# Kernel optimization log

Measured on AMD Instinct MI355X. Metric: run time of the kernel, lower is better.

## Reference

```python
import jax, jax.numpy as jnp
import numpy as np

B, N, DIM, H, DH = 8, 1024, 512, 8, 64
INNER = H * DH
SCALE = DH ** -0.5
EPS = 1e-12  # F.normalize eps


def setup_inputs() -> dict:
    key = jax.random.key(0)
    k1, k2, k3, k4, k5 = jax.random.split(key, 5)
    x = jax.random.normal(k1, (B, N, DIM), dtype=jnp.float32)
    spd = jax.random.normal(k2, (B, 1, N, N), dtype=jnp.float32)
    # per-head binomial keep mask (one realized draw of the original loop), guaranteed nonzero
    a = np.random.RandomState(0).binomial(1, 0.9, size=H)
    if a.sum() == 0:
        a[0] = 1
    head_mask = jnp.asarray(a, dtype=jnp.float32)
    W_qkv = jax.random.normal(k3, (DIM, 3 * INNER), dtype=jnp.float32) * (DIM ** -0.5)
    W_out = jax.random.normal(k4, (INNER, DIM), dtype=jnp.float32) * (INNER ** -0.5)
    b_out = jax.random.normal(k5, (DIM,), dtype=jnp.float32) * 0.01
    return {"x": x, "spd": spd, "head_mask": head_mask,
            "W_qkv": W_qkv, "W_out": W_out, "b_out": b_out}


def reference(x, spd, head_mask, W_qkv, W_out, b_out):
    b, n, _ = x.shape
    qkv = x @ W_qkv                                   # [b, n, 3*inner]
    q, k, v = jnp.split(qkv, 3, axis=-1)
    split_heads = lambda t: t.reshape(b, n, H, DH).transpose(0, 2, 1, 3)  # b h n d
    q, k, v = split_heads(q), split_heads(k), split_heads(v)

    dots = jnp.einsum('bhnd,bhmd->bhnm', q, k) * SCALE        # [b,h,n,n]
    prod = dots * spd                                         # broadcast spd over heads
    prod_norm = jnp.sqrt(jnp.sum(prod * prod, axis=-1, keepdims=True))
    dots_norm = jnp.sqrt(jnp.sum(dots * dots, axis=-1, keepdims=True))
    bias = prod / jnp.maximum(prod_norm, EPS) * dots_norm     # F.normalize(prod)*||dots||
    attn = jax.nn.softmax(dots + bias, axis=-1)

    # head dropout mask with rescale: attn * mask * H / sum(mask)
    scale_m = head_mask * (H / jnp.sum(head_mask))
    attn = attn * scale_m[None, :, None, None]

    out = jnp.einsum('bhnm,bhmd->bhnd', attn, v)              # [b,h,n,d]
    out = out.transpose(0, 2, 1, 3).reshape(b, n, INNER)      # b n (h d)
    return out @ W_out + b_out
```

## Files before the change

kernel.cpp:

```cpp
#include <hip/hip_runtime.h>
#include <hip/hip_bf16.h>

typedef __attribute__((ext_vector_type(8))) short short8;
typedef __attribute__((ext_vector_type(4))) short s16x4;
typedef __attribute__((ext_vector_type(4))) float f32x4;
typedef __attribute__((ext_vector_type(2))) _Float16 h2;

typedef const __attribute__((address_space(1))) unsigned* gp1;
typedef __attribute__((address_space(3))) unsigned* lp3;

__device__ inline short f2bf(float f) {
    union { float f; unsigned u; } v; v.f = f;
    unsigned r = v.u + 0x7fffu + ((v.u >> 16) & 1u);
    return (short)(r >> 16);
}

__global__ __launch_bounds__(256) void cvt_bf16(
    const float* __restrict__ src, short* __restrict__ dst, int n4)
{
    int i = blockIdx.x * 256 + threadIdx.x;
    if (i < n4) {
        float4 v = ((const float4*)src)[i];
        s16x4 o = { f2bf(v.x), f2bf(v.y), f2bf(v.z), f2bf(v.w) };
        ((s16x4*)dst)[i] = o;
    }
}

__global__ __launch_bounds__(256) void tr_w(
    const float* __restrict__ src, short* __restrict__ dst, int K, int N)
{
    __shared__ float t[64][65];
    const int k0 = blockIdx.x * 64, n0 = blockIdx.y * 64;
    const int r = threadIdx.x >> 4, c4 = (threadIdx.x & 15) * 4;
#pragma unroll
    for (int j = 0; j < 4; j++) {
        float4 v = *(const float4*)(src + (size_t)(k0 + r + 16 * j) * N + n0 + c4);
        t[r + 16 * j][c4 + 0] = v.x; t[r + 16 * j][c4 + 1] = v.y;
        t[r + 16 * j][c4 + 2] = v.z; t[r + 16 * j][c4 + 3] = v.w;
    }
    __syncthreads();
#pragma unroll
    for (int j = 0; j < 4; j++) {
        const int n = r + 16 * j;
        s16x4 o = { f2bf(t[c4 + 0][n]), f2bf(t[c4 + 1][n]),
                    f2bf(t[c4 + 2][n]), f2bf(t[c4 + 3][n]) };
        *(s16x4*)(dst + (size_t)(n0 + n) * K + k0 + c4) = o;
    }
}

__global__ __launch_bounds__(256) void qkv_gemm(
    const short* __restrict__ A, const short* __restrict__ BT,
    short* __restrict__ q, short* __restrict__ k, short* __restrict__ vt)
{
    __shared__ short sA[128][32];
    __shared__ short sB[128][32];

    const int tid  = threadIdx.x;
    const int wv   = tid >> 6, lane = tid & 63;
    const int quad = lane >> 4, l16 = lane & 15;
    const int wr = wv >> 1, wc = wv & 1;
    const int m0 = blockIdx.x * 128, n0 = blockIdx.y * 128;

    f32x4 acc[4][4];
#pragma unroll
    for (int i = 0; i < 4; i++)
#pragma unroll
        for (int j = 0; j < 4; j++) acc[i][j] = (f32x4){0.f, 0.f, 0.f, 0.f};

    const short* a_src = A  + (size_t)(m0 + wv * 32 + (lane >> 2)) * 512 + (lane & 3) * 8;
    const short* b_src = BT + (size_t)(n0 + wv * 32 + (lane >> 2)) * 512 + (lane & 3) * 8;
    char* a_dst = (char*)sA + wv * 2048;
    char* b_dst = (char*)sB + wv * 2048;

    for (int ks = 0; ks < 16; ks++) {
        __syncthreads();
        const short* ap = a_src + ks * 32;
        const short* bp = b_src + ks * 32;
        __builtin_amdgcn_global_load_lds((gp1)(ap),            (lp3)(a_dst),        16, 0, 0);
        __builtin_amdgcn_global_load_lds((gp1)(ap + 16 * 512), (lp3)(a_dst + 1024), 16, 0, 0);
        __builtin_amdgcn_global_load_lds((gp1)(bp),            (lp3)(b_dst),        16, 0, 0);
        __builtin_amdgcn_global_load_lds((gp1)(bp + 16 * 512), (lp3)(b_dst + 1024), 16, 0, 0);
        __syncthreads();

        short8 af[4], bf[4];
#pragma unroll
        for (int f = 0; f < 4; f++) {
            af[f] = *(const short8*)&sA[wr * 64 + f * 16 + l16][quad * 8];
            bf[f] = *(const short8*)&sB[wc * 64 + f * 16 + l16][quad * 8];
        }
#pragma unroll
        for (int fm = 0; fm < 4; fm++)
#pragma unroll
            for (int fn = 0; fn < 4; fn++)
                acc[fm][fn] = __builtin_amdgcn_mfma_f32_16x16x32_bf16(
                    af[fm], bf[fn], acc[fm][fn], 0, 0, 0);
    }

    const int sec = n0 >> 9;
#pragma unroll
    for (int fn = 0; fn < 4; fn++) {
        const int gc = n0 + wc * 64 + fn * 16 + l16;
        const int cc = gc & 511;
        const int h = cc >> 6, d = cc & 63;
#pragma unroll
        for (int fm = 0; fm < 4; fm++)
#pragma unroll
            for (int i = 0; i < 4; i++) {
                const int gm = m0 + wr * 64 + fm * 16 + quad * 4 + i;
                const int b = gm >> 10, n = gm & 1023;
                const int bh = b * 8 + h;
                if (sec == 0)      q[((size_t)(bh * 1024 + n)) * 64 + d] = f2bf(acc[fm][fn][i] * 0.125f);
                else if (sec == 1) k[((size_t)(bh * 1024 + n)) * 64 + d] = f2bf(acc[fm][fn][i]);
                else               vt[((size_t)(bh * 64 + d)) * 1024 + n] = f2bf(acc[fm][fn][i]);
            }
    }
}

__global__ __launch_bounds__(256, 3) void attn_k(
    const short* __restrict__ q, const short* __restrict__ kk,
    const short* __restrict__ vt, const float* __restrict__ spd,
    const float* __restrict__ hm, short* __restrict__ o)
{
    __shared__ short sP[16][1032];
    __shared__ float sred[4][4][16];

    const int tid  = threadIdx.x;
    const int wv   = tid >> 6, lane = tid & 63;
    const int quad = lane >> 4, l16 = lane & 15;
    const int qt = blockIdx.x, bh = blockIdx.y;
    const int b = bh >> 3, h = bh & 7;
    const int q0 = qt * 16;

    const short* qb = q + ((size_t)bh * 1024 + q0 + l16) * 64;
    short8 aq0 = *(const short8*)(qb + quad * 8);
    short8 aq1 = *(const short8*)(qb + 32 + quad * 8);

    f32x4 acc[16];
#pragma unroll
    for (int t = 0; t < 16; t++) acc[t] = (f32x4){0.f, 0.f, 0.f, 0.f};

    const short* kbh = kk + (size_t)bh * 1024 * 64;
    const float* spdb = spd + ((size_t)b * 1024 + q0 + quad * 4) * 1024;

    h2 svp[16][2];

    float svfA[8][4];
#pragma unroll
    for (int t = 0; t < 8; t++) {
        const float* sp = spdb + wv * 256 + t * 16 + l16;
        svfA[t][0] = sp[0];    svfA[t][1] = sp[1024];
        svfA[t][2] = sp[2048]; svfA[t][3] = sp[3072];
    }
#pragma unroll
    for (int t = 0; t < 8; t++) {
        const short* kb = kbh + (size_t)(wv * 256 + t * 16 + l16) * 64;
        short8 b0 = *(const short8*)(kb + quad * 8);
        short8 b1 = *(const short8*)(kb + 32 + quad * 8);
        acc[t] = __builtin_amdgcn_mfma_f32_16x16x32_bf16(aq0, b0, acc[t], 0, 0, 0);
        acc[t] = __builtin_amdgcn_mfma_f32_16x16x32_bf16(aq1, b1, acc[t], 0, 0, 0);
    }
#pragma unroll
    for (int t = 0; t < 8; t++) {
        svp[t][0] = (h2){(_Float16)svfA[t][0], (_Float16)svfA[t][1]};
        svp[t][1] = (h2){(_Float16)svfA[t][2], (_Float16)svfA[t][3]};
    }
    float svfB[8][4];
#pragma unroll
    for (int t = 0; t < 8; t++) {
        const float* sp = spdb + wv * 256 + (t + 8) * 16 + l16;
        svfB[t][0] = sp[0];    svfB[t][1] = sp[1024];
        svfB[t][2] = sp[2048]; svfB[t][3] = sp[3072];
    }
#pragma unroll
    for (int t = 8; t < 16; t++) {
        const short* kb = kbh + (size_t)(wv * 256 + t * 16 + l16) * 64;
        short8 b0 = *(const short8*)(kb + quad * 8);
        short8 b1 = *(const short8*)(kb + 32 + quad * 8);
        acc[t] = __builtin_amdgcn_mfma_f32_16x16x32_bf16(aq0, b0, acc[t], 0, 0, 0);
        acc[t] = __builtin_amdgcn_mfma_f32_16x16x32_bf16(aq1, b1, acc[t], 0, 0, 0);
    }
#pragma unroll
    for (int t = 0; t < 8; t++) {
        svp[t + 8][0] = (h2){(_Float16)svfB[t][0], (_Float16)svfB[t][1]};
        svp[t + 8][1] = (h2){(_Float16)svfB[t][2], (_Float16)svfB[t][3]};
    }

    float dn[4] = {0.f, 0.f, 0.f, 0.f}, pn[4] = {0.f, 0.f, 0.f, 0.f};
#pragma unroll
    for (int t = 0; t < 16; t++)
#pragma unroll
        for (int i = 0; i < 4; i++) {
            float s  = acc[t][i];
            float sv = (float)svp[t][i >> 1][i & 1];
            float ps = s * sv;
            dn[i] += s * s;
            pn[i] += ps * ps;
        }
#pragma unroll
    for (int m = 1; m < 16; m <<= 1)
#pragma unroll
        for (int i = 0; i < 4; i++) {
            dn[i] += __shfl_xor(dn[i], m, 64);
            pn[i] += __shfl_xor(pn[i], m, 64);
        }
    if (l16 == 0)
#pragma unroll
        for (int i = 0; i < 4; i++) {
            sred[0][wv][quad * 4 + i] = dn[i];
            sred[1][wv][quad * 4 + i] = pn[i];
        }
    __syncthreads();
    float ratio[4];
#pragma unroll
    for (int i = 0; i < 4; i++) {
        const int row = quad * 4 + i;
        float d = sred[0][0][row] + sred[0][1][row] + sred[0][2][row] + sred[0][3][row];
        float p = sred[1][0][row] + sred[1][1][row] + sred[1][2][row] + sred[1][3][row];
        ratio[i] = sqrtf(d) / fmaxf(sqrtf(p), 1e-12f);
    }

    float mx[4] = {-1e30f, -1e30f, -1e30f, -1e30f};
#pragma unroll
    for (int t = 0; t < 16; t++)
#pragma unroll
        for (int i = 0; i < 4; i++) {
            float s  = acc[t][i];
            float sv = (float)svp[t][i >> 1][i & 1];
            float l  = s * fmaf(sv, ratio[i], 1.0f);
            acc[t][i] = l;
            mx[i] = fmaxf(mx[i], l);
        }
#pragma unroll
    for (int m = 1; m < 16; m <<= 1)
#pragma unroll
        for (int i = 0; i < 4; i++) mx[i] = fmaxf(mx[i], __shfl_xor(mx[i], m, 64));
    if (l16 == 0)
#pragma unroll
        for (int i = 0; i < 4; i++) sred[2][wv][quad * 4 + i] = mx[i];
    __syncthreads();
    float mrow[4];
#pragma unroll
    for (int i = 0; i < 4; i++) {
        const int row = quad * 4 + i;
        mrow[i] = fmaxf(fmaxf(sred[2][0][row], sred[2][1][row]),
                        fmaxf(sred[2][2][row], sred[2][3][row]));
    }

    float rs[4] = {0.f, 0.f, 0.f, 0.f};
#pragma unroll
    for (int t = 0; t < 16; t++)
#pragma unroll
        for (int i = 0; i < 4; i++) {
            float p = __expf(acc[t][i] - mrow[i]);
            acc[t][i] = p;
            rs[i] += p;
        }
#pragma unroll
    for (int m = 1; m < 16; m <<= 1)
#pragma unroll
        for (int i = 0; i < 4; i++) rs[i] += __shfl_xor(rs[i], m, 64);
    if (l16 == 0)
#pragma unroll
        for (int i = 0; i < 4; i++) sred[3][wv][quad * 4 + i] = rs[i];
    __syncthreads();
    const float hsum = hm[0] + hm[1] + hm[2] + hm[3] + hm[4] + hm[5] + hm[6] + hm[7];
    const float hscale = hm[h] * 8.0f / hsum;
    float rinv[4];
#pragma unroll
    for (int i = 0; i < 4; i++) {
        const int row = quad * 4 + i;
        float s = sred[3][0][row] + sred[3][1][row] + sred[3][2][row] + sred[3][3][row];
        rinv[i] = hscale / s;
    }

#pragma unroll
    for (int t = 0; t < 16; t++) {
        const int col = wv * 256 + t * 16 + l16;
#pragma unroll
        for (int i = 0; i < 4; i++)
            sP[quad * 4 + i][col] = f2bf(acc[t][i] * rinv[i]);
    }
    __syncthreads();

    f32x4 oacc = (f32x4){0.f, 0.f, 0.f, 0.f};
    const short* vb = vt + ((size_t)bh * 64 + wv * 16 + l16) * 1024;
#pragma unroll
    for (int kkk = 0; kkk < 32; kkk++) {
        short8 pa = *(const short8*)&sP[l16][kkk * 32 + quad * 8];
        short8 vf = *(const short8*)(vb + kkk * 32 + quad * 8);
        oacc = __builtin_amdgcn_mfma_f32_16x16x32_bf16(pa, vf, oacc, 0, 0, 0);
    }
#pragma unroll
    for (int i = 0; i < 4; i++)
        o[((size_t)(b * 1024 + q0 + quad * 4 + i)) * 512 + h * 64 + wv * 16 + l16]
            = f2bf(oacc[i]);
}

__global__ __launch_bounds__(256) void out_gemm(
    const short* __restrict__ A, const short* __restrict__ BT,
    const float* __restrict__ bias, float* __restrict__ out)
{
    __shared__ short sA[128][32];
    __shared__ short sB[128][32];

    const int tid  = threadIdx.x;
    const int wv   = tid >> 6, lane = tid & 63;
    const int quad = lane >> 4, l16 = lane & 15;
    const int wr = wv >> 1, wc = wv & 1;
    const int m0 = blockIdx.x * 128, n0 = blockIdx.y * 128;

    f32x4 acc[4][4];
#pragma unroll
    for (int i = 0; i < 4; i++)
#pragma unroll
        for (int j = 0; j < 4; j++) acc[i][j] = (f32x4){0.f, 0.f, 0.f, 0.f};

    const short* a_src = A  + (size_t)(m0 + wv * 32 + (lane >> 2)) * 512 + (lane & 3) * 8;
    const short* b_src = BT + (size_t)(n0 + wv * 32 + (lane >> 2)) * 512 + (lane & 3) * 8;
    char* a_dst = (char*)sA + wv * 2048;
    char* b_dst = (char*)sB + wv * 2048;

    for (int ks = 0; ks < 16; ks++) {
        __syncthreads();
        const short* ap = a_src + ks * 32;
        const short* bp = b_src + ks * 32;
        __builtin_amdgcn_global_load_lds((gp1)(ap),            (lp3)(a_dst),        16, 0, 0);
        __builtin_amdgcn_global_load_lds((gp1)(ap + 16 * 512), (lp3)(a_dst + 1024), 16, 0, 0);
        __builtin_amdgcn_global_load_lds((gp1)(bp),            (lp3)(b_dst),        16, 0, 0);
        __builtin_amdgcn_global_load_lds((gp1)(bp + 16 * 512), (lp3)(b_dst + 1024), 16, 0, 0);
        __syncthreads();

        short8 af[4], bf[4];
#pragma unroll
        for (int f = 0; f < 4; f++) {
            af[f] = *(const short8*)&sA[wr * 64 + f * 16 + l16][quad * 8];
            bf[f] = *(const short8*)&sB[wc * 64 + f * 16 + l16][quad * 8];
        }
#pragma unroll
        for (int fm = 0; fm < 4; fm++)
#pragma unroll
            for (int fn = 0; fn < 4; fn++)
                acc[fm][fn] = __builtin_amdgcn_mfma_f32_16x16x32_bf16(
                    af[fm], bf[fn], acc[fm][fn], 0, 0, 0);
    }

#pragma unroll
    for (int fn = 0; fn < 4; fn++) {
        const int gc = n0 + wc * 64 + fn * 16 + l16;
        const float bv = bias[gc];
#pragma unroll
        for (int fm = 0; fm < 4; fm++)
#pragma unroll
            for (int i = 0; i < 4; i++) {
                const int gm = m0 + wr * 64 + fm * 16 + quad * 4 + i;
                out[(size_t)gm * 512 + gc] = acc[fm][fn][i] + bv;
            }
    }
}

extern "C" void kernel_launch(void* const* d_in, const int* in_sizes, int n_in,
                              void* d_out, int out_size, void* d_ws, size_t ws_size,
                              hipStream_t stream) {
    const float* x    = (const float*)d_in[0];
    const float* spd  = (const float*)d_in[1];
    const float* hm   = (const float*)d_in[2];
    const float* Wqkv = (const float*)d_in[3];
    const float* Wout = (const float*)d_in[4];
    const float* bout = (const float*)d_in[5];
    float* out = (float*)d_out;

    char* ws = (char*)d_ws;
    short* qw  = (short*)(ws);
    short* kw  = (short*)(ws + ((size_t)8  << 20));
    short* vtw = (short*)(ws + ((size_t)16 << 20));
    short* ow  = (short*)(ws + ((size_t)24 << 20));
    short* xb  = (short*)(ws + ((size_t)32 << 20));
    short* wqT = (short*)(ws + ((size_t)40 << 20));
    short* woT = (short*)(ws + ((size_t)42 << 20));

    cvt_bf16<<<4096, 256, 0, stream>>>(x, xb, 8192 * 512 / 4);
    tr_w    <<<dim3(8, 24), 256, 0, stream>>>(Wqkv, wqT, 512, 1536);
    tr_w    <<<dim3(8, 8),  256, 0, stream>>>(Wout, woT, 512, 512);

    qkv_gemm<<<dim3(64, 12), 256, 0, stream>>>(xb, wqT, qw, kw, vtw);
    attn_k  <<<dim3(64, 64), 256, 0, stream>>>(qw, kw, vtw, spd, hm, ow);
    out_gemm<<<dim3(64, 4),  256, 0, stream>>>(ow, woT, bout, out);
}
```

Baseline: 275.9 us.

## Transpose score MFMA layout, halve P shared buffer, vectorize spd loads

Swaps the MFMA operand order so each lane holds four consecutive key columns for one query row. This allows float4 loads of spd, single-value row reductions with two cross-quad shuffles instead of 4×4 per-row shuffle trees, and packed 8-byte stores of P into shared memory. The P staging buffer is halved and filled in two phases (waves 0-1 then waves 2-3), with extra barriers between them. The smaller shared-memory footprint is paired with raising the launch-bounds occupancy hint from 3 to 4 blocks, at the cost of two more syncs and possible register pressure.

After: 344.5 us. 24.9% more time.

```diff
diff --git a/kernel.cpp b/kernel.cpp
--- a/kernel.cpp
+++ b/kernel.cpp
@@ -116,12 +116,12 @@
     }
 }
 
-__global__ __launch_bounds__(256, 3) void attn_k(
+__global__ __launch_bounds__(256, 4) void attn_k(
     const short* __restrict__ q, const short* __restrict__ kk,
     const short* __restrict__ vt, const float* __restrict__ spd,
     const float* __restrict__ hm, short* __restrict__ o)
 {
-    __shared__ short sP[16][1032];
+    __shared__ short sP[16][520];
     __shared__ float sred[4][4][16];
 
     const int tid  = threadIdx.x;
@@ -140,52 +140,44 @@
     for (int t = 0; t < 16; t++) acc[t] = (f32x4){0.f, 0.f, 0.f, 0.f};
 
     const short* kbh = kk + (size_t)bh * 1024 * 64;
-    const float* spdb = spd + ((size_t)b * 1024 + q0 + quad * 4) * 1024;
+    const float* spdl = spd + ((size_t)b * 1024 + q0 + l16) * 1024 + wv * 256 + quad * 4;
 
     h2 svp[16][2];
-
-    float svfA[8][4];
-#pragma unroll
-    for (int t = 0; t < 8; t++) {
-        const float* sp = spdb + wv * 256 + t * 16 + l16;
-        svfA[t][0] = sp[0];    svfA[t][1] = sp[1024];
-        svfA[t][2] = sp[2048]; svfA[t][3] = sp[3072];
-    }
-#pragma unroll
-    for (int t = 0; t < 8; t++) {
-        const short* kb = kbh + (size_t)(wv * 256 + t * 16 + l16) * 64;
-        short8 b0 = *(const short8*)(kb + quad * 8);
-        short8 b1 = *(const short8*)(kb + 32 + quad * 8);
-        acc[t] = __builtin_amdgcn_mfma_f32_16x16x32_bf16(aq0, b0, acc[t], 0, 0, 0);
-        acc[t] = __builtin_amdgcn_mfma_f32_16x16x32_bf16(aq1, b1, acc[t], 0, 0, 0);
-    }
-#pragma unroll
-    for (int t = 0; t < 8; t++) {
-        svp[t][0] = (h2){(_Float16)svfA[t][0], (_Float16)svfA[t][1]};
-        svp[t][1] = (h2){(_Float16)svfA[t][2], (_Float16)svfA[t][3]};
-    }
-    float svfB[8][4];
-#pragma unroll
-    for (int t = 0; t < 8; t++) {
-        const float* sp = spdb + wv * 256 + (t + 8) * 16 + l16;
-        svfB[t][0] = sp[0];    svfB[t][1] = sp[1024];
-        svfB[t][2] = sp[2048]; svfB[t][3] = sp[3072];
-    }
-#pragma unroll
-    for (int t = 8; t < 16; t++) {
-        const short* kb = kbh + (size_t)(wv * 256 + t * 16 + l16) * 64;
-        short8 b0 = *(const short8*)(kb + quad * 8);
-        short8 b1 = *(const short8*)(kb + 32 + quad * 8);
-        acc[t] = __builtin_amdgcn_mfma_f32_16x16x32_bf16(aq0, b0, acc[t], 0, 0, 0);
-        acc[t] = __builtin_amdgcn_mfma_f32_16x16x32_bf16(aq1, b1, acc[t], 0, 0, 0);
-    }
-#pragma unroll
-    for (int t = 0; t < 8; t++) {
-        svp[t + 8][0] = (h2){(_Float16)svfB[t][0], (_Float16)svfB[t][1]};
-        svp[t + 8][1] = (h2){(_Float16)svfB[t][2], (_Float16)svfB[t][3]};
-    }
-
-    float dn[4] = {0.f, 0.f, 0.f, 0.f}, pn[4] = {0.f, 0.f, 0.f, 0.f};
+    {
+        float4 svf[8];
+#pragma unroll
+        for (int t = 0; t < 8; t++) svf[t] = *(const float4*)(spdl + t * 16);
+#pragma unroll
+        for (int t = 0; t < 8; t++) {
+            const short* kb = kbh + (size_t)(wv * 256 + t * 16 + l16) * 64;
+            short8 b0 = *(const short8*)(kb + quad * 8);
+            short8 b1 = *(const short8*)(kb + 32 + quad * 8);
+            acc[t] = __builtin_amdgcn_mfma_f32_16x16x32_bf16(b0, aq0, acc[t], 0, 0, 0);
+            acc[t] = __builtin_amdgcn_mfma_f32_16x16x32_bf16(b1, aq1, acc[t], 0, 0, 0);
+        }
+#pragma unroll
+        for (int t = 0; t < 8; t++) {
+            svp[t][0] = (h2){(_Float16)svf[t].x, (_Float16)svf[t].y};
+            svp[t][1] = (h2){(_Float16)svf[t].z, (_Float16)svf[t].w};
+        }
+#pragma unroll
+        for (int t = 0; t < 8; t++) svf[t] = *(const float4*)(spdl + (t + 8) * 16);
+#pragma unroll
+        for (int t = 8; t < 16; t++) {
+            const short* kb = kbh + (size_t)(wv * 256 + t * 16 + l16) * 64;
+            short8 b0 = *(const short8*)(kb + quad * 8);
+            short8 b1 = *(const short8*)(kb + 32 + quad * 8);
+            acc[t] = __builtin_amdgcn_mfma_f32_16x16x32_bf16(b0, aq0, acc[t], 0, 0, 0);
+            acc[t] = __builtin_amdgcn_mfma_f32_16x16x32_bf16(b1, aq1, acc[t], 0, 0, 0);
+        }
+#pragma unroll
+        for (int t = 0; t < 8; t++) {
+            svp[t + 8][0] = (h2){(_Float16)svf[t].x, (_Float16)svf[t].y};
+            svp[t + 8][1] = (h2){(_Float16)svf[t].z, (_Float16)svf[t].w};
+        }
+    }
+
+    float dn = 0.f, pn = 0.f;
 #pragma unroll
     for (int t = 0; t < 16; t++)
 #pragma unroll
@@ -193,103 +185,88 @@
             float s  = acc[t][i];
             float sv = (float)svp[t][i >> 1][i & 1];
             float ps = s * sv;
-            dn[i] += s * s;
-            pn[i] += ps * ps;
-        }
-#pragma unroll
-    for (int m = 1; m < 16; m <<= 1)
-#pragma unroll
-        for (int i = 0; i < 4; i++) {
-            dn[i] += __shfl_xor(dn[i], m, 64);
-            pn[i] += __shfl_xor(pn[i], m, 64);
-        }
-    if (l16 == 0)
-#pragma unroll
-        for (int i = 0; i < 4; i++) {
-            sred[0][wv][quad * 4 + i] = dn[i];
-            sred[1][wv][quad * 4 + i] = pn[i];
-        }
-    __syncthreads();
-    float ratio[4];
-#pragma unroll
-    for (int i = 0; i < 4; i++) {
-        const int row = quad * 4 + i;
-        float d = sred[0][0][row] + sred[0][1][row] + sred[0][2][row] + sred[0][3][row];
-        float p = sred[1][0][row] + sred[1][1][row] + sred[1][2][row] + sred[1][3][row];
-        ratio[i] = sqrtf(d) / fmaxf(sqrtf(p), 1e-12f);
-    }
-
-    float mx[4] = {-1e30f, -1e30f, -1e30f, -1e30f};
+            dn = fmaf(s, s, dn);
+            pn = fmaf(ps, ps, pn);
+        }
+    dn += __shfl_xor(dn, 16, 64); dn += __shfl_xor(dn, 32, 64);
+    pn += __shfl_xor(pn, 16, 64); pn += __shfl_xor(pn, 32, 64);
+    if (quad == 0) { sred[0][wv][l16] = dn; sred[1][wv][l16] = pn; }
+    __syncthreads();
+    float dtot = sred[0][0][l16] + sred[0][1][l16] + sred[0][2][l16] + sred[0][3][l16];
+    float ptot = sred[1][0][l16] + sred[1][1][l16] + sred[1][2][l16] + sred[1][3][l16];
+    const float ratio = sqrtf(dtot) / fmaxf(sqrtf(ptot), 1e-12f);
+
+    float mx = -1e30f;
 #pragma unroll
     for (int t = 0; t < 16; t++)
 #pragma unroll
         for (int i = 0; i < 4; i++) {
             float s  = acc[t][i];
             float sv = (float)svp[t][i >> 1][i & 1];
-            float l  = s * fmaf(sv, ratio[i], 1.0f);
+            float l  = s * fmaf(sv, ratio, 1.0f);
             acc[t][i] = l;
-            mx[i] = fmaxf(mx[i], l);
-        }
-#pragma unroll
-    for (int m = 1; m < 16; m <<= 1)
-#pragma unroll
-        for (int i = 0; i < 4; i++) mx[i] = fmaxf(mx[i], __shfl_xor(mx[i], m, 64));
-    if (l16 == 0)
-#pragma unroll
-        for (int i = 0; i < 4; i++) sred[2][wv][quad * 4 + i] = mx[i];
-    __syncthreads();
-    float mrow[4];
-#pragma unroll
-    for (int i = 0; i < 4; i++) {
-        const int row = quad * 4 + i;
-        mrow[i] = fmaxf(fmaxf(sred[2][0][row], sred[2][1][row]),
-                        fmaxf(sred[2][2][row], sred[2][3][row]));
-    }
-
-    float rs[4] = {0.f, 0.f, 0.f, 0.f};
+            mx = fmaxf(mx, l);
+        }
+    mx = fmaxf(mx, __shfl_xor(mx, 16, 64));
+    mx = fmaxf(mx, __shfl_xor(mx, 32, 64));
+    if (quad == 0) sred[2][wv][l16] = mx;
+    __syncthreads();
+    const float mrow = fmaxf(fmaxf(sred[2][0][l16], sred[2][1][l16]),
+                             fmaxf(sred[2][2][l16], sred[2][3][l16]));
+
+    float rs = 0.f;
 #pragma unroll
     for (int t = 0; t < 16; t++)
 #pragma unroll
         for (int i = 0; i < 4; i++) {
-            float p = __expf(acc[t][i] - mrow[i]);
+            float p = __expf(acc[t][i] - mrow);
             acc[t][i] = p;
-            rs[i] += p;
-        }
-#pragma unroll
-    for (int m = 1; m < 16; m <<= 1)
-#pragma unroll
-        for (int i = 0; i < 4; i++) rs[i] += __shfl_xor(rs[i], m, 64);
-    if (l16 == 0)
-#pragma unroll
-        for (int i = 0; i < 4; i++) sred[3][wv][quad * 4 + i] = rs[i];
+            rs += p;
+        }
+    rs += __shfl_xor(rs, 16, 64); rs += __shfl_xor(rs, 32, 64);
+    if (quad == 0) sred[3][wv][l16] = rs;
     __syncthreads();
     const float hsum = hm[0] + hm[1] + hm[2] + hm[3] + hm[4] + hm[5] + hm[6] + hm[7];
     const float hscale = hm[h] * 8.0f / hsum;
-    float rinv[4];
-#pragma unroll
-    for (int i = 0; i < 4; i++) {
-        const int row = quad * 4 + i;
-        float s = sred[3][0][row] + sred[3][1][row] + sred[3][2][row] + sred[3][3][row];
-        rinv[i] = hscale / s;
-    }
-
-#pragma unroll
-    for (int t = 0; t < 16; t++) {
-        const int col = wv * 256 + t * 16 + l16;
-#pragma unroll
-        for (int i = 0; i < 4; i++)
-            sP[quad * 4 + i][col] = f2bf(acc[t][i] * rinv[i]);
-    }
-    __syncthreads();
-
+    const float rsum = sred[3][0][l16] + sred[3][1][l16] + sred[3][2][l16] + sred[3][3][l16];
+    const float rinv = hscale / rsum;
+
+    s16x4 pk[16];
+#pragma unroll
+    for (int t = 0; t < 16; t++)
+        pk[t] = (s16x4){ f2bf(acc[t][0] * rinv), f2bf(acc[t][1] * rinv),
+                         f2bf(acc[t][2] * rinv), f2bf(acc[t][3] * rinv) };
+
+    const short* vb = vt + ((size_t)bh * 64 + wv * 16 + l16) * 1024;
+    const int c0 = (wv & 1) * 256 + quad * 4;
     f32x4 oacc = (f32x4){0.f, 0.f, 0.f, 0.f};
-    const short* vb = vt + ((size_t)bh * 64 + wv * 16 + l16) * 1024;
-#pragma unroll
-    for (int kkk = 0; kkk < 32; kkk++) {
-        short8 pa = *(const short8*)&sP[l16][kkk * 32 + quad * 8];
-        short8 vf = *(const short8*)(vb + kkk * 32 + quad * 8);
+
+    if (wv < 2) {
+#pragma unroll
+        for (int t = 0; t < 16; t++)
+            *(s16x4*)&sP[l16][c0 + t * 16] = pk[t];
+    }
+    __syncthreads();
+#pragma unroll
+    for (int kk2 = 0; kk2 < 16; kk2++) {
+        short8 pa = *(const short8*)&sP[l16][kk2 * 32 + quad * 8];
+        short8 vf = *(const short8*)(vb + kk2 * 32 + quad * 8);
         oacc = __builtin_amdgcn_mfma_f32_16x16x32_bf16(pa, vf, oacc, 0, 0, 0);
     }
+    __syncthreads();
+    if (wv >= 2) {
+#pragma unroll
+        for (int t = 0; t < 16; t++)
+            *(s16x4*)&sP[l16][c0 + t * 16] = pk[t];
+    }
+    __syncthreads();
+#pragma unroll
+    for (int kk2 = 0; kk2 < 16; kk2++) {
+        short8 pa = *(const short8*)&sP[l16][kk2 * 32 + quad * 8];
+        short8 vf = *(const short8*)(vb + 512 + kk2 * 32 + quad * 8);
+        oacc = __builtin_amdgcn_mfma_f32_16x16x32_bf16(pa, vf, oacc, 0, 0, 0);
+    }
+
 #pragma unroll
     for (int i = 0; i < 4; i++)
         o[((size_t)(b * 1024 + q0 + quad * 4 + i)) * 512 + h * 64 + wv * 16 + l16]
```
